# Optimization experiments

Measured on AMD Instinct MI355X. Metric: run time of the kernel, lower is better.

The kernel has to match this reference:

```python
import jax, jax.numpy as jnp
import numpy as np

PAD = 1  # PAD_token; embedding rows at PAD are zero (padding_idx)


def setup_inputs() -> dict:
    V, D, HOPS = 50000, 128, 3
    B, Lc, Mc = 16, 256, 8
    Lk, Mk = 512, 8
    key = jax.random.key(0)
    kC, kK, kc, kk = jax.random.split(key, 4)
    # one table per hop (C_0..C_{HOPS-1}, K_0..K_{HOPS-1}), init N(0, 0.1)
    C = 0.1 * jax.random.normal(kC, (HOPS, V, D), dtype=jnp.float32)
    K = 0.1 * jax.random.normal(kK, (HOPS, V, D), dtype=jnp.float32)
    C = C.at[:, PAD].set(0.0)
    K = K.at[:, PAD].set(0.0)
    conv_seqs = jax.random.randint(kc, (B, Lc, Mc), 0, V)
    kb_arr = jax.random.randint(kk, (B, Lk, Mk), 0, V)  # dense, PAD-padded ragged KB
    return {"conv_seqs": conv_seqs, "kb_arr": kb_arr, "C": C, "K": K}


def reference(conv_seqs, kb_arr, C, K):
    B, Lc, _ = conv_seqs.shape
    HOPS, _, D = C.shape
    conv_feature = jnp.zeros((B, Lc, D), dtype=C.dtype)
    for hop in range(HOPS):
        # embedding-bag: gather + sum over span tokens
        cf = jnp.sum(C[hop][conv_seqs], axis=2)  # [B, Lc, D]
        kf = jnp.sum(K[hop][kb_arr], axis=2)     # [B, Lk, D]
        att = jnp.einsum('bld,bkd->blk', cf, kf)  # [B, Lc, Lk]
        p = jax.nn.softmax(att, axis=-1)
        conv_feature = jnp.einsum('blk,bkd->bld', p, kf) + conv_feature
    return conv_feature.transpose(1, 0, 2)  # [Lc, B, D]
```

## Files before the change

kernel.cpp:

```cpp
#include <hip/hip_runtime.h>

#define V_    50000
#define D_    128
#define HOPS_ 3
#define B_    16
#define LC_   256
#define MC_   8
#define LK_   512
#define MK_   8

typedef __bf16  bf16x8  __attribute__((ext_vector_type(8)));
typedef unsigned short ushort8 __attribute__((ext_vector_type(8)));
typedef float   floatx4 __attribute__((ext_vector_type(4)));

__device__ inline unsigned short f2bf(float f) {
    union { float f; unsigned u; } x; x.f = f;
    unsigned r = x.u + 0x7FFFu + ((x.u >> 16) & 1u);
    return (unsigned short)(r >> 16);
}

__device__ inline floatx4 mfma_bf16(ushort8 a, ushort8 b, floatx4 c) {
    return __builtin_amdgcn_mfma_f32_16x16x32_bf16(
        __builtin_bit_cast(bf16x8, a), __builtin_bit_cast(bf16x8, b), c, 0, 0, 0);
}

__global__ __launch_bounds__(256) void zero_kernel(float4* __restrict__ p) {
    p[(size_t)blockIdx.x * 256 + threadIdx.x] = make_float4(0.f, 0.f, 0.f, 0.f);
}

__global__ __launch_bounds__(256) void gather_kernel(
    const int* __restrict__ conv_seqs, const int* __restrict__ kb_arr,
    const float* __restrict__ Ct, const float* __restrict__ Kt,
    unsigned short* __restrict__ kf, unsigned short* __restrict__ kfT,
    unsigned short* __restrict__ cf)
{
    __shared__ float tile[32][132];

    const int tid  = threadIdx.x;
    const int r    = tid >> 3;
    const int s    = tid & 7;
    const int d0   = s * 16;
    const int lane = tid & 63;
    const int bx   = blockIdx.x;

    const int*   idxp;
    const float* table;
    unsigned short* dst;
    bool do_transpose;
    int hop, b, row0;

    constexpr int KBLK = HOPS_ * B_ * (LK_ / 32);
    if (bx < KBLK) {
        hop  = bx / (B_ * 16);
        int rem = bx % (B_ * 16);
        b    = rem >> 4;
        row0 = (rem & 15) * 32;
        idxp  = kb_arr + (size_t)(b * LK_ + row0 + r) * MK_;
        table = Kt + (size_t)hop * V_ * D_;
        dst   = kf + (((size_t)(hop * B_ + b) * LK_) + row0 + r) * D_ + d0;
        do_transpose = true;
    } else {
        int id = bx - KBLK;
        hop  = id / (B_ * 8);
        int rem = id % (B_ * 8);
        b    = rem >> 3;
        row0 = (rem & 7) * 32;
        idxp  = conv_seqs + (size_t)(b * LC_ + row0 + r) * MC_;
        table = Ct + (size_t)hop * V_ * D_;
        dst   = cf + (((size_t)(hop * B_ + b) * LC_) + row0 + r) * D_ + d0;
        do_transpose = false;
    }

    const int myidx = idxp[s];

    float4 acc[4];
    #pragma unroll
    for (int j = 0; j < 4; ++j) acc[j] = make_float4(0.f, 0.f, 0.f, 0.f);

    #pragma unroll
    for (int m = 0; m < 8; ++m) {
        int idx = __shfl(myidx, (lane & 56) + m);
        const float4* src = (const float4*)(table + (size_t)idx * D_ + d0);
        #pragma unroll
        for (int j = 0; j < 4; ++j) {
            float4 v = src[j];
            acc[j].x += v.x; acc[j].y += v.y; acc[j].z += v.z; acc[j].w += v.w;
        }
    }

    {
        ushort8 o0, o1;
        o0[0] = f2bf(acc[0].x); o0[1] = f2bf(acc[0].y);
        o0[2] = f2bf(acc[0].z); o0[3] = f2bf(acc[0].w);
        o0[4] = f2bf(acc[1].x); o0[5] = f2bf(acc[1].y);
        o0[6] = f2bf(acc[1].z); o0[7] = f2bf(acc[1].w);
        o1[0] = f2bf(acc[2].x); o1[1] = f2bf(acc[2].y);
        o1[2] = f2bf(acc[2].z); o1[3] = f2bf(acc[2].w);
        o1[4] = f2bf(acc[3].x); o1[5] = f2bf(acc[3].y);
        o1[6] = f2bf(acc[3].z); o1[7] = f2bf(acc[3].w);
        *(ushort8*)(dst)     = o0;
        *(ushort8*)(dst + 8) = o1;
    }

    if (do_transpose) {
        #pragma unroll
        for (int j = 0; j < 4; ++j)
            *(float4*)&tile[r][d0 + j * 4] = acc[j];
        __syncthreads();
        const int d    = tid >> 1;
        const int koff = (tid & 1) * 16;
        unsigned short* tdst =
            kfT + ((size_t)(hop * B_ + b) * D_ + d) * LK_ + row0 + koff;
        #pragma unroll
        for (int i0 = 0; i0 < 16; i0 += 8) {
            ushort8 o;
            #pragma unroll
            for (int i = 0; i < 8; ++i) o[i] = f2bf(tile[koff + i0 + i][d]);
            *(ushort8*)(tdst + i0) = o;
        }
    }
}

__global__ __launch_bounds__(512) void attn_kernel(
    const unsigned short* __restrict__ kf, const unsigned short* __restrict__ kfT,
    const unsigned short* __restrict__ cf, float* __restrict__ out)
{
    constexpr int AS = 516;
    __shared__ float att_s[16][AS];
    __shared__ float rowinv_s[16];

    const int tid  = threadIdx.x;
    const int wave = tid >> 6;
    const int lane = tid & 63;
    const int quad = lane >> 4;
    const int l16  = lane & 15;

    const int hop = blockIdx.x >> 8;
    const int rem = blockIdx.x & 255;
    const int b   = rem >> 4;
    const int l0  = (rem & 15) * 16;

    const unsigned short* cf_h  = cf  + (((size_t)(hop * 16 + b)) * 256 + l0) * 128;
    const unsigned short* kf_h  = kf  + ((size_t)(hop * 16 + b)) * 512 * 128;
    const unsigned short* kfT_h = kfT + ((size_t)(hop * 16 + b)) * 128 * 512;

    ushort8 afrag[4];
    #pragma unroll
    for (int ks = 0; ks < 4; ++ks)
        afrag[ks] = *(const ushort8*)(cf_h + l16 * 128 + ks * 32 + quad * 8);

    #pragma unroll
    for (int t = 0; t < 4; ++t) {
        const int nt = wave * 4 + t;
        floatx4 acc = {0.f, 0.f, 0.f, 0.f};
        #pragma unroll
        for (int ks = 0; ks < 4; ++ks) {
            ushort8 bfrag = *(const ushort8*)(kf_h + (nt * 16 + l16) * 128 + ks * 32 + quad * 8);
            acc = mfma_bf16(afrag[ks], bfrag, acc);
        }
        #pragma unroll
        for (int rr = 0; rr < 4; ++rr)
            att_s[quad * 4 + rr][nt * 16 + l16] = acc[rr];
    }
    __syncthreads();

    #pragma unroll
    for (int rr = 0; rr < 2; ++rr) {
        const int row = wave * 2 + rr;
        float v[8];
        float mx = -1e30f;
        #pragma unroll
        for (int j = 0; j < 8; ++j) {
            v[j] = att_s[row][lane + j * 64];
            mx = fmaxf(mx, v[j]);
        }
        #pragma unroll
        for (int off = 32; off; off >>= 1) mx = fmaxf(mx, __shfl_xor(mx, off));
        float sum = 0.f;
        #pragma unroll
        for (int j = 0; j < 8; ++j) {
            float e = __expf(v[j] - mx);
            att_s[row][lane + j * 64] = e;
            sum += e;
        }
        #pragma unroll
        for (int off = 32; off; off >>= 1) sum += __shfl_xor(sum, off);
        if (lane == 0) rowinv_s[row] = 1.0f / sum;
    }
    __syncthreads();

    floatx4 pacc = {0.f, 0.f, 0.f, 0.f};
    #pragma unroll
    for (int ks = 0; ks < 16; ++ks) {
        const float* prow = &att_s[l16][ks * 32 + quad * 8];
        float4 p0 = *(const float4*)(prow);
        float4 p1 = *(const float4*)(prow + 4);
        ushort8 pa;
        pa[0] = f2bf(p0.x); pa[1] = f2bf(p0.y); pa[2] = f2bf(p0.z); pa[3] = f2bf(p0.w);
        pa[4] = f2bf(p1.x); pa[5] = f2bf(p1.y); pa[6] = f2bf(p1.z); pa[7] = f2bf(p1.w);
        ushort8 bfrag = *(const ushort8*)(kfT_h + (size_t)(wave * 16 + l16) * 512 + ks * 32 + quad * 8);
        pacc = mfma_bf16(pa, bfrag, pacc);
    }

    const int d = wave * 16 + l16;
    #pragma unroll
    for (int rr = 0; rr < 4; ++rr)
        atomicAdd(&out[(((size_t)(l0 + quad * 4 + rr)) * 16 + b) * 128 + d],
                  pacc[rr] * rowinv_s[quad * 4 + rr]);
}

extern "C" void kernel_launch(void* const* d_in, const int* in_sizes, int n_in,
                              void* d_out, int out_size, void* d_ws, size_t ws_size,
                              hipStream_t stream) {
    (void)in_sizes; (void)n_in; (void)out_size; (void)ws_size;
    const int*   conv_seqs = (const int*)d_in[0];
    const int*   kb_arr    = (const int*)d_in[1];
    const float* C         = (const float*)d_in[2];
    const float* K         = (const float*)d_in[3];

    unsigned short* kf  = (unsigned short*)d_ws;
    unsigned short* kfT = kf  + (size_t)HOPS_ * B_ * LK_ * D_;
    unsigned short* cf  = kfT + (size_t)HOPS_ * B_ * LK_ * D_;
    float* out = (float*)d_out;

    hipLaunchKernelGGL(zero_kernel, dim3(512), dim3(256), 0, stream, (float4*)out);
    hipLaunchKernelGGL(gather_kernel, dim3(1152), dim3(256), 0, stream,
                       conv_seqs, kb_arr, C, K, kf, kfT, cf);
    hipLaunchKernelGGL(attn_kernel, dim3(768), dim3(512), 0, stream,
                       kf, kfT, cf, out);
}
```

Before: 198.6 us.

## Fuse output zeroing into gather kernel and remap attention blocks for XCD locality

Output zeroing now runs as extra blocks appended to the gather kernel, which drops one kernel launch. The attention kernel's block index is remapped so that blocks sharing a (hop, batch) pair land on the same XCD under round-robin dispatch. The aim is for kf/kfT reuse to hit in that XCD's L2. This relies on the hardware dispatch order, and the zero blocks add a little load imbalance to the gather grid.

After: 196.0 us. Within noise of the previous version (-1.3%).

```diff
diff --git a/kernel.cpp b/kernel.cpp
--- a/kernel.cpp
+++ b/kernel.cpp
@@ -24,24 +24,30 @@
         __builtin_bit_cast(bf16x8, a), __builtin_bit_cast(bf16x8, b), c, 0, 0, 0);
 }
 
-__global__ __launch_bounds__(256) void zero_kernel(float4* __restrict__ p) {
-    p[(size_t)blockIdx.x * 256 + threadIdx.x] = make_float4(0.f, 0.f, 0.f, 0.f);
-}
-
 __global__ __launch_bounds__(256) void gather_kernel(
     const int* __restrict__ conv_seqs, const int* __restrict__ kb_arr,
     const float* __restrict__ Ct, const float* __restrict__ Kt,
     unsigned short* __restrict__ kf, unsigned short* __restrict__ kfT,
-    unsigned short* __restrict__ cf)
+    unsigned short* __restrict__ cf, float4* __restrict__ out4)
 {
     __shared__ float tile[32][132];
 
     const int tid  = threadIdx.x;
+    const int bx   = blockIdx.x;
+
+    constexpr int KBLK = HOPS_ * B_ * (LK_ / 32);
+    constexpr int CBLK = HOPS_ * B_ * (LC_ / 32);
+
+    if (bx >= KBLK + CBLK) {
+        int zb = bx - (KBLK + CBLK);
+        out4[(size_t)zb * 256 + tid] = make_float4(0.f, 0.f, 0.f, 0.f);
+        return;
+    }
+
     const int r    = tid >> 3;
     const int s    = tid & 7;
     const int d0   = s * 16;
     const int lane = tid & 63;
-    const int bx   = blockIdx.x;
 
     const int*   idxp;
     const float* table;
@@ -49,7 +55,6 @@
     bool do_transpose;
     int hop, b, row0;
 
-    constexpr int KBLK = HOPS_ * B_ * (LK_ / 32);
     if (bx < KBLK) {
         hop  = bx / (B_ * 16);
         int rem = bx % (B_ * 16);
@@ -135,14 +140,18 @@
     const int quad = lane >> 4;
     const int l16  = lane & 15;
 
-    const int hop = blockIdx.x >> 8;
-    const int rem = blockIdx.x & 255;
-    const int b   = rem >> 4;
-    const int l0  = (rem & 15) * 16;
-
-    const unsigned short* cf_h  = cf  + (((size_t)(hop * 16 + b)) * 256 + l0) * 128;
-    const unsigned short* kf_h  = kf  + ((size_t)(hop * 16 + b)) * 512 * 128;
-    const unsigned short* kfT_h = kfT + ((size_t)(hop * 16 + b)) * 128 * 512;
+    const int gl  = blockIdx.x & 7;
+    const int s_  = blockIdx.x >> 3;
+    const int lt  = s_ / 6;
+    const int gh  = s_ % 6;
+    const int g   = gh * 8 + gl;
+    const int hop = g >> 4;
+    const int b   = g & 15;
+    const int l0  = lt * 16;
+
+    const unsigned short* cf_h  = cf  + (((size_t)g) * 256 + l0) * 128;
+    const unsigned short* kf_h  = kf  + ((size_t)g) * 512 * 128;
+    const unsigned short* kfT_h = kfT + ((size_t)g) * 128 * 512;
 
     ushort8 afrag[4];
     #pragma unroll
@@ -223,9 +232,8 @@
     unsigned short* cf  = kfT + (size_t)HOPS_ * B_ * LK_ * D_;
     float* out = (float*)d_out;
 
-    hipLaunchKernelGGL(zero_kernel, dim3(512), dim3(256), 0, stream, (float4*)out);
-    hipLaunchKernelGGL(gather_kernel, dim3(1152), dim3(256), 0, stream,
-                       conv_seqs, kb_arr, C, K, kf, kfT, cf);
+    hipLaunchKernelGGL(gather_kernel, dim3(1664), dim3(256), 0, stream,
+                       conv_seqs, kb_arr, C, K, kf, kfT, cf, (float4*)out);
     hipLaunchKernelGGL(attn_kernel, dim3(768), dim3(512), 0, stream,
                        kf, kfT, cf, out);
 }
```
